# Kernel tuning notes

Measured on AMD Instinct MI355X. Metric: run time of the kernel, lower is better.

## Reference

```python
import jax, jax.numpy as jnp
import numpy as np


def gcn_conv(x, W, b, src, dst, num_nodes):
    """PyG GCNConv with add_self_loops=True, symmetric normalization, bias.
    src/dst already include self-loops. deg computed from unit edge weights."""
    deg = jax.ops.segment_sum(jnp.ones(src.shape[0], x.dtype), dst,
                              num_segments=num_nodes)
    dinv = jnp.where(deg > 0, jax.lax.rsqrt(deg), 0.0)
    norm = dinv[src] * dinv[dst]               # [E]
    h = x @ W                                  # [N, F_out] dense GEMM first
    msg = h[src] * norm[:, None]               # gather + scale, [E, F_out]
    out = jax.ops.segment_sum(msg, dst, num_segments=num_nodes)  # scatter-add
    return out + b


def setup_inputs() -> dict:
    key = jax.random.key(0)
    ks = jax.random.split(key, 5)
    N, E, F_in, F_out = 50000, 800000, 512, 40
    x = jax.random.normal(ks[0], (N, F_in), dtype=jnp.float32)
    edge_index = jax.random.randint(ks[1], (2, E), 0, N, dtype=jnp.int64)
    W1 = jax.random.normal(ks[2], (F_in, 256), dtype=jnp.float32) * (F_in ** -0.5)
    W2 = jax.random.normal(ks[3], (256, 16), dtype=jnp.float32) * (256 ** -0.5)
    W3 = jax.random.normal(ks[4], (16, F_out), dtype=jnp.float32) * (16 ** -0.5)
    return {
        "x": x, "edge_index": edge_index,
        "W1": W1, "b1": jnp.zeros((256,), jnp.float32),
        "W2": W2, "b2": jnp.zeros((16,), jnp.float32),
        "W3": W3, "b3": jnp.zeros((F_out,), jnp.float32),
    }


def reference(x, edge_index, W1, b1, W2, b2, W3, b3):
    N = x.shape[0]
    loop = jnp.arange(N, dtype=edge_index.dtype)
    src = jnp.concatenate([edge_index[0], loop])  # self-loops appended once,
    dst = jnp.concatenate([edge_index[1], loop])  # shared by all three layers
    h = gcn_conv(x, W1, b1, src, dst, N)
    h = jax.nn.relu(h)                 # dropout is identity in eval mode
    h = gcn_conv(h, W2, b2, src, dst, N)
    h = jax.nn.relu(h)
    h = gcn_conv(h, W3, b3, src, dst, N)
    return jax.nn.log_softmax(h, axis=1)
```

## Files before the change

### kernel.cpp

```cpp
#include <hip/hip_runtime.h>
#include <hip/hip_bf16.h>
#include <math.h>

typedef __hip_bfloat16 bf16;
typedef __attribute__((ext_vector_type(8))) __bf16 bf16x8;
typedef __attribute__((ext_vector_type(4))) float f32x4;

#define KIN 512
#define F1  256
#define F2  16
#define F3  40


__device__ inline unsigned pk_bf2(float a, float b) {
  bf16 x = __float2bfloat16(a), y = __float2bfloat16(b);
  unsigned short ux = *(unsigned short*)&x, uy = *(unsigned short*)&y;
  return (unsigned)ux | ((unsigned)uy << 16);
}
__device__ inline float bfbits(unsigned u16) {
  unsigned v = u16 << 16;
  return *(float*)&v;
}
__device__ inline void async16(const void* g, void* l) {
  __builtin_amdgcn_global_load_lds((const __attribute__((address_space(1))) void*)g,
                                   (__attribute__((address_space(3))) void*)l, 16, 0, 0);
}
__device__ inline void accum8(float* acc, uint4 h, float w) {
  acc[0] = fmaf(w, bfbits(h.x & 0xffff), acc[0]);
  acc[1] = fmaf(w, bfbits(h.x >> 16),    acc[1]);
  acc[2] = fmaf(w, bfbits(h.y & 0xffff), acc[2]);
  acc[3] = fmaf(w, bfbits(h.y >> 16),    acc[3]);
  acc[4] = fmaf(w, bfbits(h.z & 0xffff), acc[4]);
  acc[5] = fmaf(w, bfbits(h.z >> 16),    acc[5]);
  acc[6] = fmaf(w, bfbits(h.w & 0xffff), acc[6]);
  acc[7] = fmaf(w, bfbits(h.w >> 16),    acc[7]);
}


__global__ __launch_bounds__(256) void k_init2(int* __restrict__ cnt,
                                               const int* __restrict__ ei, int* __restrict__ flag,
                                               const float* __restrict__ W,
                                               unsigned short* __restrict__ Wt,
                                               int n, int nb) {
  int b = blockIdx.x;
  int t = threadIdx.x;
  if (b < nb) {
    int i = b * 256 + t;
    if (i < n) cnt[i] = 0;
    if (b == 0 && t == 0)
      *flag = (ei[1] == 0 && ei[3] == 0 && ei[5] == 0 && ei[7] == 0) ? 1 : 0;
  } else {
    __shared__ float tile[32][33];
    int b2 = b - nb;
    int k0 = (b2 & 15) * 32;
    int n0 = (b2 >> 4) * 32;
    int lr = t >> 5, lc = t & 31;
#pragma unroll
    for (int rr = 0; rr < 32; rr += 8)
      tile[lr + rr][lc] = W[(size_t)(k0 + lr + rr) * F1 + n0 + lc];
    __syncthreads();
#pragma unroll
    for (int rr = 0; rr < 32; rr += 8) {
      bf16 v = __float2bfloat16(tile[lc][lr + rr]);
      Wt[(size_t)(n0 + lr + rr) * KIN + k0 + lc] = *(unsigned short*)&v;
    }
  }
}


__global__ __launch_bounds__(256) void k_count_conv(const int* __restrict__ ei,
                                                    const int* __restrict__ flag,
                                                    int* __restrict__ cnt,
                                                    int* __restrict__ rank,
                                                    int E, int nct, int stride,
                                                    const float* __restrict__ X,
                                                    unsigned short* __restrict__ Xb,
                                                    int total8) {
  int b = blockIdx.x;
  int t = threadIdx.x;
  bool is_cnt = (b % stride == 0) && (b / stride < nct);
  if (is_cnt) {
    int e = (b / stride) * 256 + t;
    if (e >= E) return;
    int is64 = *flag;
    int d = is64 ? ei[2 * E + 2 * e] : ei[E + e];
    rank[e] = atomicAdd(&cnt[d], 1);
  } else {
    int nb_before = (b + stride - 1) / stride;
    if (nb_before > nct) nb_before = nct;
    int idx = (b - nb_before) * 256 + t;
    if (idx >= total8) return;
    const float4* src = (const float4*)X + (size_t)idx * 2;
    float4 f0 = src[0], f1 = src[1];
    uint4 pk;
    pk.x = pk_bf2(f0.x, f0.y); pk.y = pk_bf2(f0.z, f0.w);
    pk.z = pk_bf2(f1.x, f1.y); pk.w = pk_bf2(f1.z, f1.w);
    ((uint4*)Xb)[idx] = pk;
  }
}

__global__ __launch_bounds__(256) void k_scan1(const int* __restrict__ cnt,
                                               int* __restrict__ off,
                                               int* __restrict__ bsum,
                                               float* __restrict__ dinv, int N) {
  __shared__ int s[256];
  int t = threadIdx.x;
  int base = blockIdx.x * 1024 + t * 4;
  int v0 = (base + 0 < N) ? cnt[base + 0] : 0;
  int v1 = (base + 1 < N) ? cnt[base + 1] : 0;
  int v2 = (base + 2 < N) ? cnt[base + 2] : 0;
  int v3 = (base + 3 < N) ? cnt[base + 3] : 0;
  if (base + 0 < N) dinv[base + 0] = rsqrtf((float)(v0 + 1));
  if (base + 1 < N) dinv[base + 1] = rsqrtf((float)(v1 + 1));
  if (base + 2 < N) dinv[base + 2] = rsqrtf((float)(v2 + 1));
  if (base + 3 < N) dinv[base + 3] = rsqrtf((float)(v3 + 1));
  int tsum = v0 + v1 + v2 + v3;
  s[t] = tsum;
  __syncthreads();
  for (int d = 1; d < 256; d <<= 1) {
    int u = (t >= d) ? s[t - d] : 0;
    __syncthreads();
    s[t] += u;
    __syncthreads();
  }
  int excl = s[t] - tsum;
  int p0 = excl + v0, p1 = p0 + v1, p2 = p1 + v2, p3 = p2 + v3;
  if (base + 0 < N) off[base + 1] = p0;
  if (base + 1 < N) off[base + 2] = p1;
  if (base + 2 < N) off[base + 3] = p2;
  if (base + 3 < N) off[base + 4] = p3;
  if (t == 255) bsum[blockIdx.x] = s[255];
}

__global__ void k_scan2(const int* __restrict__ bsum, int* __restrict__ carry, int nb) {
  int t = threadIdx.x;
  int v = (t < nb) ? bsum[t] : 0;
  int incl = v;
  for (int d = 1; d < 64; d <<= 1) {
    int u = __shfl_up(incl, d, 64);
    if (t >= d) incl += u;
  }
  if (t < nb) carry[t] = incl - v;
}

__global__ __launch_bounds__(256) void k_scan3(int* __restrict__ off,
                                               const int* __restrict__ carry, int N) {
  int t = threadIdx.x;
  int c = carry[blockIdx.x];
  int base = blockIdx.x * 1024 + t * 4;
#pragma unroll
  for (int k = 0; k < 4; ++k)
    if (base + k < N) off[base + k + 1] += c;
  if (blockIdx.x == 0 && t == 0) off[0] = 0;
}

__global__ void k_scatter(const int* __restrict__ ei, const int* __restrict__ flag,
                          const int* __restrict__ off, const int* __restrict__ rank,
                          const float* __restrict__ dinv,
                          int2* __restrict__ ew, int E) {
  int e = blockIdx.x * 256 + threadIdx.x;
  if (e >= E) return;
  int is64 = *flag;
  int s, d;
  if (is64) { s = ei[2 * e]; d = ei[2 * E + 2 * e]; }
  else      { s = ei[e];     d = ei[E + e]; }
  int pos = off[d] + rank[e];
  float w = dinv[s] * dinv[d];
  ew[pos] = make_int2(s, __float_as_int(w));
}


__global__ __launch_bounds__(256) void k_gemm1(const unsigned short* __restrict__ Ab,
                                               const unsigned short* __restrict__ Bt,
                                               bf16* __restrict__ C, int M) {
  __shared__ unsigned short As[128 * 32];
  __shared__ unsigned short Bs[128 * 32];
  int t = threadIdx.x;
  int wave = t >> 6, lane = t & 63;
  int wm = wave >> 1, wn = wave & 1;
  int row0 = blockIdx.x * 128, col0 = blockIdx.y * 128;
  int q = lane >> 4, m16 = lane & 15;
  int srow = lane >> 2, schk = lane & 3;

  f32x4 acc[4][4];
#pragma unroll
  for (int i = 0; i < 4; ++i)
#pragma unroll
    for (int j = 0; j < 4; ++j) acc[i][j] = {0.f, 0.f, 0.f, 0.f};

  for (int kb = 0; kb < 16; ++kb) {
    __syncthreads();
#pragma unroll
    for (int jj = 0; jj < 2; ++jj) {
      int lr = wave * 32 + jj * 16 + srow;
      int gr = row0 + lr; if (gr >= M) gr = M - 1;
      int gchk = schk ^ ((lr >> 1) & 3);
      async16(Ab + (size_t)gr * KIN + kb * 32 + gchk * 8,
              As + (wave * 32 + jj * 16) * 32);
    }
#pragma unroll
    for (int jj = 0; jj < 2; ++jj) {
      int lr = wave * 32 + jj * 16 + srow;
      int gchk = schk ^ ((lr >> 1) & 3);
      async16(Bt + (size_t)(col0 + lr) * KIN + kb * 32 + gchk * 8,
              Bs + (wave * 32 + jj * 16) * 32);
    }
    __syncthreads();
    bf16x8 af[4], bfr[4];
#pragma unroll
    for (int i = 0; i < 4; ++i) {
      int m = wm * 64 + i * 16 + m16;
      af[i] = *(const bf16x8*)(As + m * 32 + ((q ^ ((m >> 1) & 3)) * 8));
    }
#pragma unroll
    for (int j = 0; j < 4; ++j) {
      int n = wn * 64 + j * 16 + m16;
      bfr[j] = *(const bf16x8*)(Bs + n * 32 + ((q ^ ((n >> 1) & 3)) * 8));
    }
#pragma unroll
    for (int j = 0; j < 4; ++j)
#pragma unroll
      for (int i = 0; i < 4; ++i)
        acc[i][j] = __builtin_amdgcn_mfma_f32_16x16x32_bf16(af[i], bfr[j], acc[i][j], 0, 0, 0);
  }

#pragma unroll
  for (int i = 0; i < 4; ++i) {
#pragma unroll
    for (int r = 0; r < 4; ++r) {
      int row = row0 + wm * 64 + i * 16 + q * 4 + r;
      if (row < M) {
#pragma unroll
        for (int j = 0; j < 4; ++j) {
          int col = col0 + wn * 64 + j * 16 + m16;
          C[(size_t)row * F1 + col] = __float2bfloat16(acc[i][j][r]);
        }
      }
    }
  }
}


__global__ __launch_bounds__(256) void k_agg1(const bf16* __restrict__ H,
                                              const int* __restrict__ off,
                                              const int2* __restrict__ ew,
                                              const float* __restrict__ dinv,
                                              const float* __restrict__ bias,
                                              bf16* __restrict__ O, int N) {
  int t = threadIdx.x;
  int i = blockIdx.x * 8 + (t >> 5);
  if (i >= N) return;
  int f0 = (t & 31) * 8;
  const unsigned short* Hu = (const unsigned short*)H;
  float di = dinv[i];
  float w0 = di * di;
  float acc[8];
  {
    uint4 h = *(const uint4*)(Hu + (size_t)i * F1 + f0);
    acc[0] = w0 * bfbits(h.x & 0xffff); acc[1] = w0 * bfbits(h.x >> 16);
    acc[2] = w0 * bfbits(h.y & 0xffff); acc[3] = w0 * bfbits(h.y >> 16);
    acc[4] = w0 * bfbits(h.z & 0xffff); acc[5] = w0 * bfbits(h.z >> 16);
    acc[6] = w0 * bfbits(h.w & 0xffff); acc[7] = w0 * bfbits(h.w >> 16);
  }
  int e = off[i], e1 = off[i + 1];
  for (; e + 8 <= e1; e += 8) {
    int2 p0 = ew[e + 0], p1 = ew[e + 1], p2 = ew[e + 2], p3 = ew[e + 3];
    int2 p4 = ew[e + 4], p5 = ew[e + 5], p6 = ew[e + 6], p7 = ew[e + 7];
    uint4 g0 = *(const uint4*)(Hu + (size_t)p0.x * F1 + f0);
    uint4 g1 = *(const uint4*)(Hu + (size_t)p1.x * F1 + f0);
    uint4 g2 = *(const uint4*)(Hu + (size_t)p2.x * F1 + f0);
    uint4 g3 = *(const uint4*)(Hu + (size_t)p3.x * F1 + f0);
    uint4 g4 = *(const uint4*)(Hu + (size_t)p4.x * F1 + f0);
    uint4 g5 = *(const uint4*)(Hu + (size_t)p5.x * F1 + f0);
    uint4 g6 = *(const uint4*)(Hu + (size_t)p6.x * F1 + f0);
    uint4 g7 = *(const uint4*)(Hu + (size_t)p7.x * F1 + f0);
    accum8(acc, g0, __int_as_float(p0.y));
    accum8(acc, g1, __int_as_float(p1.y));
    accum8(acc, g2, __int_as_float(p2.y));
    accum8(acc, g3, __int_as_float(p3.y));
    accum8(acc, g4, __int_as_float(p4.y));
    accum8(acc, g5, __int_as_float(p5.y));
    accum8(acc, g6, __int_as_float(p6.y));
    accum8(acc, g7, __int_as_float(p7.y));
  }
  for (; e < e1; ++e) {
    int2 pe = ew[e];
    uint4 g = *(const uint4*)(Hu + (size_t)pe.x * F1 + f0);
    accum8(acc, g, __int_as_float(pe.y));
  }
  float4 b0 = *(const float4*)(bias + f0);
  float4 b1 = *(const float4*)(bias + f0 + 4);
  float bb[8] = {b0.x, b0.y, b0.z, b0.w, b1.x, b1.y, b1.z, b1.w};
  uint4 o;
  unsigned* op = (unsigned*)&o;
#pragma unroll
  for (int k = 0; k < 4; ++k) {
    float lo = fmaxf(acc[2 * k] + bb[2 * k], 0.f);
    float hi = fmaxf(acc[2 * k + 1] + bb[2 * k + 1], 0.f);
    op[k] = pk_bf2(lo, hi);
  }
  *(uint4*)((unsigned short*)O + (size_t)i * F1 + f0) = o;
}


__global__ __launch_bounds__(256) void k_gemm2(const bf16* __restrict__ A,
                                               const float* __restrict__ W,
                                               float* __restrict__ C, int N) {
  __shared__ float Ws[F1 * F2];
  __shared__ float Ts[16][F1];
  int t = threadIdx.x;
  int r0 = blockIdx.x * 16;
#pragma unroll
  for (int j = 0; j < 16; ++j) Ws[t + 256 * j] = W[t + 256 * j];
  const unsigned short* Au = (const unsigned short*)A;
#pragma unroll
  for (int j = 0; j < 2; ++j) {
    int idx = t + 256 * j;
    int r = idx >> 5;
    int c8 = (idx & 31) * 8;
    int row = r0 + r;
    uint4 g = make_uint4(0, 0, 0, 0);
    if (row < N) g = *(const uint4*)(Au + (size_t)row * F1 + c8);
    float* ts = &Ts[r][c8];
    ts[0] = bfbits(g.x & 0xffff); ts[1] = bfbits(g.x >> 16);
    ts[2] = bfbits(g.y & 0xffff); ts[3] = bfbits(g.y >> 16);
    ts[4] = bfbits(g.z & 0xffff); ts[5] = bfbits(g.z >> 16);
    ts[6] = bfbits(g.w & 0xffff); ts[7] = bfbits(g.w >> 16);
  }
  __syncthreads();
  int r = t >> 4, c = t & 15;
  float acc = 0.f;
  const float4* tv = (const float4*)&Ts[r][0];
#pragma unroll 8
  for (int k4 = 0; k4 < 64; ++k4) {
    float4 a = tv[k4];
    int k = k4 * 4;
    acc = fmaf(a.x, Ws[(k + 0) * 16 + c], acc);
    acc = fmaf(a.y, Ws[(k + 1) * 16 + c], acc);
    acc = fmaf(a.z, Ws[(k + 2) * 16 + c], acc);
    acc = fmaf(a.w, Ws[(k + 3) * 16 + c], acc);
  }
  int row = r0 + r;
  if (row < N) C[(size_t)row * F2 + c] = acc;
}


__global__ __launch_bounds__(256) void k_agg16(const float* __restrict__ H,
                                               const int* __restrict__ off,
                                               const int2* __restrict__ ew,
                                               const float* __restrict__ dinv,
                                               const float* __restrict__ bias,
                                               float* __restrict__ O, int N) {
  int t = threadIdx.x;
  int i = blockIdx.x * 16 + (t >> 4);
  int f = t & 15;
  if (i >= N) return;
  float di = dinv[i];
  float acc = di * di * H[(size_t)i * F2 + f];
  int e = off[i], e1 = off[i + 1];
  for (; e + 4 <= e1; e += 4) {
    int2 p0 = ew[e + 0], p1 = ew[e + 1], p2 = ew[e + 2], p3 = ew[e + 3];
    float g0 = H[(size_t)p0.x * F2 + f];
    float g1 = H[(size_t)p1.x * F2 + f];
    float g2 = H[(size_t)p2.x * F2 + f];
    float g3 = H[(size_t)p3.x * F2 + f];
    acc = fmaf(__int_as_float(p0.y), g0, acc);
    acc = fmaf(__int_as_float(p1.y), g1, acc);
    acc = fmaf(__int_as_float(p2.y), g2, acc);
    acc = fmaf(__int_as_float(p3.y), g3, acc);
  }
  for (; e < e1; ++e) {
    int2 pe = ew[e];
    acc = fmaf(__int_as_float(pe.y), H[(size_t)pe.x * F2 + f], acc);
  }
  acc = fmaxf(acc + bias[f], 0.f);
  O[(size_t)i * F2 + f] = acc;
}


__global__ __launch_bounds__(256) void k_agg3_g3(const float* __restrict__ H,
                                                 const int* __restrict__ off,
                                                 const int2* __restrict__ ew,
                                                 const float* __restrict__ dinv,
                                                 const float* __restrict__ W3,
                                                 const float* __restrict__ b3,
                                                 float* __restrict__ O, int N) {
  __shared__ float W3s[F2 * F3];
  __shared__ float b3s[F3];
  __shared__ float aggs[16 * 17];
  int t = threadIdx.x;
  for (int idx = t; idx < F2 * F3; idx += 256) W3s[idx] = W3[idx];
  if (t < F3) b3s[t] = b3[t];
  __syncthreads();

  int node = t >> 4, f = t & 15;
  int i = blockIdx.x * 16 + node;
  if (i >= N) return;
  float di = dinv[i];
  float acc = di * di * H[(size_t)i * F2 + f];
  int e = off[i], e1 = off[i + 1];
  for (; e + 4 <= e1; e += 4) {
    int2 p0 = ew[e + 0], p1 = ew[e + 1], p2 = ew[e + 2], p3 = ew[e + 3];
    float g0 = H[(size_t)p0.x * F2 + f];
    float g1 = H[(size_t)p1.x * F2 + f];
    float g2 = H[(size_t)p2.x * F2 + f];
    float g3 = H[(size_t)p3.x * F2 + f];
    acc = fmaf(__int_as_float(p0.y), g0, acc);
    acc = fmaf(__int_as_float(p1.y), g1, acc);
    acc = fmaf(__int_as_float(p2.y), g2, acc);
    acc = fmaf(__int_as_float(p3.y), g3, acc);
  }
  for (; e < e1; ++e) {
    int2 pe = ew[e];
    acc = fmaf(__int_as_float(pe.y), H[(size_t)pe.x * F2 + f], acc);
  }
  aggs[node * 17 + f] = acc;

  const float* ar = &aggs[node * 17];
  float o0 = b3s[f], o1 = b3s[f + 16], o2 = (f < 8) ? b3s[f + 32] : 0.f;
#pragma unroll
  for (int k = 0; k < F2; ++k) {
    float a = ar[k];
    o0 = fmaf(a, W3s[k * F3 + f], o0);
    o1 = fmaf(a, W3s[k * F3 + f + 16], o1);
    if (f < 8) o2 = fmaf(a, W3s[k * F3 + f + 32], o2);
  }
  float m = fmaxf(o0, o1);
  if (f < 8) m = fmaxf(m, o2);
#pragma unroll
  for (int d = 1; d < 16; d <<= 1) m = fmaxf(m, __shfl_xor(m, d, 16));
  float s = __expf(o0 - m) + __expf(o1 - m) + ((f < 8) ? __expf(o2 - m) : 0.f);
#pragma unroll
  for (int d = 1; d < 16; d <<= 1) s += __shfl_xor(s, d, 16);
  float lse = m + __logf(s);
  float* orow = O + (size_t)i * F3;
  orow[f] = o0 - lse;
  orow[f + 16] = o1 - lse;
  if (f < 8) orow[f + 32] = o2 - lse;
}


extern "C" void kernel_launch(void* const* d_in, const int* in_sizes, int n_in,
                              void* d_out, int out_size, void* d_ws, size_t ws_size,
                              hipStream_t stream) {
  const float* x  = (const float*)d_in[0];
  const int*   ei = (const int*)d_in[1];
  const float* W1 = (const float*)d_in[2];
  const float* b1 = (const float*)d_in[3];
  const float* W2 = (const float*)d_in[4];
  const float* b2 = (const float*)d_in[5];
  const float* W3 = (const float*)d_in[6];
  const float* b3 = (const float*)d_in[7];
  float* out = (float*)d_out;

  int N = in_sizes[0] / KIN;
  int E = in_sizes[1] / 2;

  char* p = (char*)d_ws;
  auto take = [&](size_t bytes) {
    char* r = p;
    p += (bytes + 255) & ~(size_t)255;
    return r;
  };
  int*   flag  = (int*)take(4);
  int*   cnt   = (int*)take((size_t)N * 4);
  int*   off   = (int*)take((size_t)(N + 1) * 4);
  float* dinv  = (float*)take((size_t)N * 4);
  int*   bsum  = (int*)take(64 * 4);
  int*   carry = (int*)take(64 * 4);
  int*   rank  = (int*)take((size_t)E * 4);
  int2*  ew    = (int2*)take((size_t)E * 8);
  unsigned short* w1t = (unsigned short*)take((size_t)KIN * F1 * 2);
  unsigned short* xb  = (unsigned short*)take((size_t)N * KIN * 2);
  bf16*  h1    = (bf16*)take((size_t)N * F1 * 2);
  bf16*  out1  = (bf16*)take((size_t)N * F1 * 2);
  float* h2    = (float*)take((size_t)N * F2 * 4);
  float* out2  = (float*)take((size_t)N * F2 * 4);

  int nb  = (N + 255) / 256;
  int ebk = (E + 255) / 256;
  int nsc = (N + 1023) / 1024;
  int total8 = (N * KIN) / 8;
  int cvb = (total8 + 255) / 256;
  int tot = ebk + cvb;
  int stride = tot / ebk; if (stride < 1) stride = 1;

  k_init2<<<nb + 128, 256, 0, stream>>>(cnt, ei, flag, W1, w1t, N, nb);
  k_count_conv<<<tot, 256, 0, stream>>>(ei, flag, cnt, rank, E, ebk, stride, x, xb, total8);
  k_scan1<<<nsc, 256, 0, stream>>>(cnt, off, bsum, dinv, N);
  k_scan2<<<1, 64, 0, stream>>>(bsum, carry, nsc);
  k_scan3<<<nsc, 256, 0, stream>>>(off, carry, N);
  k_scatter<<<ebk, 256, 0, stream>>>(ei, flag, off, rank, dinv, ew, E);

  dim3 g1((N + 127) / 128, F1 / 128);
  k_gemm1<<<g1, 256, 0, stream>>>(xb, w1t, h1, N);
  k_agg1<<<(N + 7) / 8, 256, 0, stream>>>(h1, off, ew, dinv, b1, out1, N);
  k_gemm2<<<(N + 15) / 16, 256, 0, stream>>>(out1, W2, h2, N);
  k_agg16<<<(N + 15) / 16, 256, 0, stream>>>(h2, off, ew, dinv, b2, out2, N);
  k_agg3_g3<<<(N + 15) / 16, 256, 0, stream>>>(out2, off, ew, dinv, W3, b3, out, N);
}
```

Measured before the change: 357.3 us.

## Merge scan kernels, fuse edge scatter into GEMM1 launch, split agg1 by feature halves

Folds the block-carry scan into the scan-apply kernel, where each block reduces its predecessor block sums with a wave shuffle. The edge scatter now runs as extra blocks in the GEMM1 launch so the two overlap, and k_agg1 is split into two feature halves with 16 threads per node. This removes two launches and aims to improve cache locality in the layer-1 gather. The gather half-split rereads edge lists twice, and the GEMM blocks now use a 1D block index mapping.

Measured after the change: 348.3 us. -2.5%, faster.

```diff
diff --git a/kernel.cpp b/kernel.cpp
--- a/kernel.cpp
+++ b/kernel.cpp
@@ -132,21 +132,17 @@
   if (t == 255) bsum[blockIdx.x] = s[255];
 }
 
-__global__ void k_scan2(const int* __restrict__ bsum, int* __restrict__ carry, int nb) {
-  int t = threadIdx.x;
-  int v = (t < nb) ? bsum[t] : 0;
-  int incl = v;
-  for (int d = 1; d < 64; d <<= 1) {
-    int u = __shfl_up(incl, d, 64);
-    if (t >= d) incl += u;
-  }
-  if (t < nb) carry[t] = incl - v;
-}
-
-__global__ __launch_bounds__(256) void k_scan3(int* __restrict__ off,
-                                               const int* __restrict__ carry, int N) {
-  int t = threadIdx.x;
-  int c = carry[blockIdx.x];
+__global__ __launch_bounds__(256) void k_scan3m(int* __restrict__ off,
+                                                const int* __restrict__ bsum, int N) {
+  __shared__ int cs;
+  int t = threadIdx.x;
+  if (t < 64) {
+    int v = (t < blockIdx.x) ? bsum[t] : 0;
+    for (int d = 32; d; d >>= 1) v += __shfl_xor(v, d, 64);
+    if (t == 0) cs = v;
+  }
+  __syncthreads();
+  int c = cs;
   int base = blockIdx.x * 1024 + t * 4;
 #pragma unroll
   for (int k = 0; k < 4; ++k)
@@ -154,31 +150,36 @@
   if (blockIdx.x == 0 && t == 0) off[0] = 0;
 }
 
-__global__ void k_scatter(const int* __restrict__ ei, const int* __restrict__ flag,
-                          const int* __restrict__ off, const int* __restrict__ rank,
-                          const float* __restrict__ dinv,
-                          int2* __restrict__ ew, int E) {
-  int e = blockIdx.x * 256 + threadIdx.x;
-  if (e >= E) return;
-  int is64 = *flag;
-  int s, d;
-  if (is64) { s = ei[2 * e]; d = ei[2 * E + 2 * e]; }
-  else      { s = ei[e];     d = ei[E + e]; }
-  int pos = off[d] + rank[e];
-  float w = dinv[s] * dinv[d];
-  ew[pos] = make_int2(s, __float_as_int(w));
-}
-
-
-__global__ __launch_bounds__(256) void k_gemm1(const unsigned short* __restrict__ Ab,
-                                               const unsigned short* __restrict__ Bt,
-                                               bf16* __restrict__ C, int M) {
+
+__global__ __launch_bounds__(256) void k_gemm1_sc(const unsigned short* __restrict__ Ab,
+                                                  const unsigned short* __restrict__ Bt,
+                                                  bf16* __restrict__ C, int M, int ngx,
+                                                  const int* __restrict__ ei,
+                                                  const int* __restrict__ flag,
+                                                  const int* __restrict__ off,
+                                                  const int* __restrict__ rank,
+                                                  const float* __restrict__ dinv,
+                                                  int2* __restrict__ ew, int E) {
   __shared__ unsigned short As[128 * 32];
   __shared__ unsigned short Bs[128 * 32];
-  int t = threadIdx.x;
+  int b = blockIdx.x;
+  int t = threadIdx.x;
+  int ngemm = ngx * 2;
+  if (b >= ngemm) {
+    int e = (b - ngemm) * 256 + t;
+    if (e >= E) return;
+    int is64 = *flag;
+    int s, d;
+    if (is64) { s = ei[2 * e]; d = ei[2 * E + 2 * e]; }
+    else      { s = ei[e];     d = ei[E + e]; }
+    int pos = off[d] + rank[e];
+    float w = dinv[s] * dinv[d];
+    ew[pos] = make_int2(s, __float_as_int(w));
+    return;
+  }
   int wave = t >> 6, lane = t & 63;
   int wm = wave >> 1, wn = wave & 1;
-  int row0 = blockIdx.x * 128, col0 = blockIdx.y * 128;
+  int row0 = (b % ngx) * 128, col0 = (b / ngx) * 128;
   int q = lane >> 4, m16 = lane & 15;
   int srow = lane >> 2, schk = lane & 3;
 
@@ -246,11 +247,14 @@
                                               const int2* __restrict__ ew,
                                               const float* __restrict__ dinv,
                                               const float* __restrict__ bias,
-                                              bf16* __restrict__ O, int N) {
-  int t = threadIdx.x;
-  int i = blockIdx.x * 8 + (t >> 5);
+                                              bf16* __restrict__ O, int N, int nbb) {
+  int b = blockIdx.x;
+  int t = threadIdx.x;
+  int phase = (b >= nbb) ? 1 : 0;
+  int b2 = b - phase * nbb;
+  int i = b2 * 16 + (t >> 4);
   if (i >= N) return;
-  int f0 = (t & 31) * 8;
+  int f0 = phase * 128 + (t & 15) * 8;
   const unsigned short* Hu = (const unsigned short*)H;
   float di = dinv[i];
   float w0 = di * di;
@@ -467,7 +471,6 @@
   int*   off   = (int*)take((size_t)(N + 1) * 4);
   float* dinv  = (float*)take((size_t)N * 4);
   int*   bsum  = (int*)take(64 * 4);
-  int*   carry = (int*)take(64 * 4);
   int*   rank  = (int*)take((size_t)E * 4);
   int2*  ew    = (int2*)take((size_t)E * 8);
   unsigned short* w1t = (unsigned short*)take((size_t)KIN * F1 * 2);
@@ -488,13 +491,14 @@
   k_init2<<<nb + 128, 256, 0, stream>>>(cnt, ei, flag, W1, w1t, N, nb);
   k_count_conv<<<tot, 256, 0, stream>>>(ei, flag, cnt, rank, E, ebk, stride, x, xb, total8);
   k_scan1<<<nsc, 256, 0, stream>>>(cnt, off, bsum, dinv, N);
-  k_scan2<<<1, 64, 0, stream>>>(bsum, carry, nsc);
-  k_scan3<<<nsc, 256, 0, stream>>>(off, carry, N);
-  k_scatter<<<ebk, 256, 0, stream>>>(ei, flag, off, rank, dinv, ew, E);
-
-  dim3 g1((N + 127) / 128, F1 / 128);
-  k_gemm1<<<g1, 256, 0, stream>>>(xb, w1t, h1, N);
-  k_agg1<<<(N + 7) / 8, 256, 0, stream>>>(h1, off, ew, dinv, b1, out1, N);
+  k_scan3m<<<nsc, 256, 0, stream>>>(off, bsum, N);
+
+  int ngx = (N + 127) / 128;
+  k_gemm1_sc<<<ngx * 2 + ebk, 256, 0, stream>>>(xb, w1t, h1, N, ngx,
+                                                ei, flag, off, rank, dinv, ew, E);
+
+  int nbb = (N + 15) / 16;
+  k_agg1<<<nbb * 2, 256, 0, stream>>>(h1, off, ew, dinv, b1, out1, N, nbb);
   k_gemm2<<<(N + 15) / 16, 256, 0, stream>>>(out1, W2, h2, N);
   k_agg16<<<(N + 15) / 16, 256, 0, stream>>>(h2, off, ew, dinv, b2, out2, N);
   k_agg3_g3<<<(N + 15) / 16, 256, 0, stream>>>(out2, off, ew, dinv, W3, b3, out, N);
```
